# Optimization experiments

Hardware: AMD Instinct MI355X
Metric: run time of the kernel (lower is better)

Reference implementation:

```python
import jax, jax.numpy as jnp
import numpy as np

N = 50000          # nodes
E = 800000         # edges
D_IN, D_HID, D_OUT = 256, 128, 64
NUM_GRAPHS = 16
BN_EPS = 1e-5


def gcn_conv(x, src, dst, W, b, n_nodes):
    """PyG GCNConv: add self-loops, sym-normalized aggregation, then bias."""
    loop = jnp.arange(n_nodes, dtype=src.dtype)
    s = jnp.concatenate([src, loop])
    d = jnp.concatenate([dst, loop])
    deg = jax.ops.segment_sum(jnp.ones_like(s, dtype=x.dtype), d, num_segments=n_nodes)
    dinv = jax.lax.rsqrt(jnp.maximum(deg, 1.0))  # deg >= 1 due to self-loops
    norm = dinv[s] * dinv[d]                      # [E+N]
    h = x @ W                                     # [N, out]
    msg = h[s] * norm[:, None]                    # gather + scale
    out = jax.ops.segment_sum(msg, d, num_segments=n_nodes)
    return out + b


def batch_norm(x, gamma, beta):
    mu = jnp.mean(x, axis=0)
    var = jnp.mean(jnp.square(x - mu), axis=0)
    return (x - mu) * jax.lax.rsqrt(var + BN_EPS) * gamma + beta


def setup_inputs() -> dict:
    key = jax.random.key(0)
    ks = jax.random.split(key, 10)
    x = jax.random.normal(ks[0], (N, D_IN), dtype=jnp.float32)
    edge_index = jax.random.randint(ks[1], (2, E), 0, N, dtype=jnp.int64)
    batch = jnp.sort(jax.random.randint(ks[2], (N,), 0, NUM_GRAPHS, dtype=jnp.int64))
    def glorot(k, fan_in, fan_out):
        lim = np.sqrt(6.0 / (fan_in + fan_out))
        return jax.random.uniform(k, (fan_in, fan_out), jnp.float32, -lim, lim)
    return {
        "x": x, "edge_index": edge_index, "batch": batch,
        "W1": glorot(ks[3], D_IN, D_HID),  "b1": jnp.zeros((D_HID,), jnp.float32),
        "W2": glorot(ks[4], D_HID, D_HID), "b2": jnp.zeros((D_HID,), jnp.float32),
        "W3": glorot(ks[5], D_HID, D_OUT), "b3": jnp.zeros((D_OUT,), jnp.float32),
        "g1": jnp.ones((D_HID,), jnp.float32), "be1": jnp.zeros((D_HID,), jnp.float32),
        "g2": jnp.ones((D_HID,), jnp.float32), "be2": jnp.zeros((D_HID,), jnp.float32),
    }


def reference(x, edge_index, batch, W1, b1, W2, b2, W3, b3, g1, be1, g2, be2):
    src, dst = edge_index[0], edge_index[1]
    n = x.shape[0]
    h = gcn_conv(x, src, dst, W1, b1, n)
    h = jax.nn.relu(batch_norm(h, g1, be1))
    h = gcn_conv(h, src, dst, W2, b2, n)
    h = jax.nn.relu(batch_norm(h, g2, be2))
    h = gcn_conv(h, src, dst, W3, b3, n)          # [N, D_OUT]
    # global mean pool over graph ids
    sums = jax.ops.segment_sum(h, batch, num_segments=NUM_GRAPHS)
    cnts = jax.ops.segment_sum(jnp.ones((n,), h.dtype), batch, num_segments=NUM_GRAPHS)
    return sums / jnp.maximum(cnts, 1.0)[:, None]  # [NUM_GRAPHS, D_OUT]
```

## Files before the change

kernel.cpp:

```cpp
#include <hip/hip_runtime.h>
#include <hip/hip_bf16.h>

#define D_IN   256
#define D_HID  128
#define D_OUT_ 64
#define NGRAPH 16
#define BN_EPS 1e-5f

#define SCAN_TPB 256
#define SCAN_VPT 4

typedef __attribute__((ext_vector_type(8))) short short8;
typedef __attribute__((ext_vector_type(4))) float floatx4;

__device__ __forceinline__ unsigned short f2bf(float x) {
    unsigned u = __float_as_uint(x);
    return (unsigned short)((u + 0x7fffu + ((u >> 16) & 1u)) >> 16);
}
__device__ __forceinline__ unsigned pack2bf(float lo, float hi) {
    return (unsigned)f2bf(lo) | ((unsigned)f2bf(hi) << 16);
}
__device__ __forceinline__ void bf2_decode(unsigned u, float& lo, float& hi) {
    lo = __uint_as_float(u << 16);
    hi = __uint_as_float(u & 0xffff0000u);
}
__device__ __forceinline__ void accum8(float* acc, uint4 qv, float wt) {
    float f0,f1,f2,f3,f4,f5,f6,f7;
    bf2_decode(qv.x, f0, f1); bf2_decode(qv.y, f2, f3);
    bf2_decode(qv.z, f4, f5); bf2_decode(qv.w, f6, f7);
    acc[0]=fmaf(f0,wt,acc[0]); acc[1]=fmaf(f1,wt,acc[1]);
    acc[2]=fmaf(f2,wt,acc[2]); acc[3]=fmaf(f3,wt,acc[3]);
    acc[4]=fmaf(f4,wt,acc[4]); acc[5]=fmaf(f5,wt,acc[5]);
    acc[6]=fmaf(f6,wt,acc[6]); acc[7]=fmaf(f7,wt,acc[7]);
}

__global__ void count_rank_kernel(const int* __restrict__ dst, int E,
                                  int* __restrict__ deg, int* __restrict__ rank) {
    int e = blockIdx.x * blockDim.x + threadIdx.x;
    if (e < E) rank[e] = atomicAdd(&deg[dst[e]], 1);
}

__global__ void dinv_bsum_kernel(const int* __restrict__ deg, int N,
                                 float* __restrict__ dinv, int* __restrict__ bsum) {
    __shared__ int red[SCAN_TPB];
    int t = threadIdx.x;
    int base = blockIdx.x * (SCAN_TPB * SCAN_VPT) + t;
    int s = 0;
    #pragma unroll
    for (int i = 0; i < SCAN_VPT; ++i) {
        int idx = base + i * SCAN_TPB;
        if (idx < N) {
            int d = deg[idx];
            dinv[idx] = rsqrtf((float)(d + 1));
            s += d;
        }
    }
    red[t] = s;
    __syncthreads();
    for (int off = SCAN_TPB / 2; off > 0; off >>= 1) {
        if (t < off) red[t] += red[t + off];
        __syncthreads();
    }
    if (t == 0) bsum[blockIdx.x] = red[0];
}

__global__ void scan_bsum_kernel(const int* __restrict__ bsum, int NB,
                                 int* __restrict__ bprefix,
                                 int* __restrict__ rowstart, int N, int E) {
    __shared__ int part[SCAN_TPB];
    int t = threadIdx.x;
    int s = (t < NB) ? bsum[t] : 0;
    part[t] = s;
    __syncthreads();
    for (int off = 1; off < SCAN_TPB; off <<= 1) {
        int x = (t >= off) ? part[t - off] : 0;
        __syncthreads();
        part[t] += x;
        __syncthreads();
    }
    if (t < NB) bprefix[t] = part[t] - s;
    if (t == 0) rowstart[N] = E;
}

__global__ void local_scan_kernel(const int* __restrict__ deg, int N,
                                  const int* __restrict__ bprefix,
                                  int* __restrict__ rowstart) {
    __shared__ int part[SCAN_TPB];
    int t = threadIdx.x;
    int base = blockIdx.x * (SCAN_TPB * SCAN_VPT) + t * SCAN_VPT;
    int v[SCAN_VPT];
    int s = 0;
    #pragma unroll
    for (int i = 0; i < SCAN_VPT; ++i) {
        v[i] = (base + i < N) ? deg[base + i] : 0;
        s += v[i];
    }
    part[t] = s;
    __syncthreads();
    for (int off = 1; off < SCAN_TPB; off <<= 1) {
        int x = (t >= off) ? part[t - off] : 0;
        __syncthreads();
        part[t] += x;
        __syncthreads();
    }
    int excl = part[t] - s + bprefix[blockIdx.x];
    #pragma unroll
    for (int i = 0; i < SCAN_VPT; ++i) {
        if (base + i < N) rowstart[base + i] = excl;
        excl += v[i];
    }
}

__global__ void wprep_all_kernel(const float* __restrict__ W1, const float* __restrict__ W2,
                                 const float* __restrict__ W3,
                                 unsigned short* __restrict__ Wt1,
                                 unsigned short* __restrict__ Wt2,
                                 unsigned short* __restrict__ Wt3) {
    int idx = blockIdx.x * blockDim.x + threadIdx.x;
    const int S1 = D_IN * D_HID;
    const int S2 = D_HID * D_HID;
    const int S3 = D_HID * D_OUT_;
    if (idx < S1) {
        int k = idx / D_HID, n = idx - k * D_HID;
        Wt1[(size_t)n * D_IN + k] = f2bf(W1[idx]);
    } else if (idx < S1 + S2) {
        int i = idx - S1;
        int k = i / D_HID, n = i - k * D_HID;
        Wt2[(size_t)n * D_HID + k] = f2bf(W2[i]);
    } else if (idx < S1 + S2 + S3) {
        int i = idx - S1 - S2;
        int k = i / D_OUT_, n = i - k * D_OUT_;
        Wt3[(size_t)n * D_HID + k] = f2bf(W3[i]);
    }
}

template<int K, int NOUT, int FUSE, int ABF16>
__device__ __forceinline__ void gemm_body(
        int bid, const void* __restrict__ Aptr, const unsigned short* __restrict__ Wt,
        unsigned short* __restrict__ Cb, int M,
        const float* __restrict__ sums, const float* __restrict__ sumsq,
        const float* __restrict__ gam, const float* __restrict__ bet, float invN) {
    constexpr int NT = NOUT / 16;
    constexpr int KS = K / 32;
    __shared__ float s_sc[FUSE ? K : 1];
    __shared__ float s_sh[FUSE ? K : 1];
    if (FUSE) {
        int t = threadIdx.x;
        if (t < K) {
            float mu  = sums[t] * invN;
            float var = sumsq[t] * invN - mu * mu;
            float sc  = gam[t] * rsqrtf(var + BN_EPS);
            s_sc[t] = sc;
            s_sh[t] = fmaf(-mu, sc, bet[t]);
        }
        __syncthreads();
    }
    int lane = threadIdx.x & 63;
    int wave = threadIdx.x >> 6;
    int col  = lane & 15;
    int quad = lane >> 4;
    int kq   = quad * 8;
    int row  = bid * 64 + wave * 16 + col;
    int rowc = min(row, M - 1);

    short8 afr[KS];
    if (ABF16) {
        const unsigned short* Ab = (const unsigned short*)Aptr;
        uint4 q[KS];
        #pragma unroll
        for (int i = 0; i < KS; ++i)
            q[i] = *(const uint4*)&Ab[(size_t)rowc * K + i * 32 + kq];
        __builtin_amdgcn_sched_barrier(0);
        #pragma unroll
        for (int i = 0; i < KS; ++i) {
            if (FUSE) {
                int kb = i * 32 + kq;
                float f0,f1,f2,f3,f4,f5,f6,f7;
                bf2_decode(q[i].x, f0, f1); bf2_decode(q[i].y, f2, f3);
                bf2_decode(q[i].z, f4, f5); bf2_decode(q[i].w, f6, f7);
                float4 sc0 = *(const float4*)&s_sc[kb];
                float4 sc1 = *(const float4*)&s_sc[kb + 4];
                float4 sh0 = *(const float4*)&s_sh[kb];
                float4 sh1 = *(const float4*)&s_sh[kb + 4];
                f0 = fmaxf(0.f, fmaf(f0, sc0.x, sh0.x));
                f1 = fmaxf(0.f, fmaf(f1, sc0.y, sh0.y));
                f2 = fmaxf(0.f, fmaf(f2, sc0.z, sh0.z));
                f3 = fmaxf(0.f, fmaf(f3, sc0.w, sh0.w));
                f4 = fmaxf(0.f, fmaf(f4, sc1.x, sh1.x));
                f5 = fmaxf(0.f, fmaf(f5, sc1.y, sh1.y));
                f6 = fmaxf(0.f, fmaf(f6, sc1.z, sh1.z));
                f7 = fmaxf(0.f, fmaf(f7, sc1.w, sh1.w));
                uint4 p;
                p.x = pack2bf(f0, f1); p.y = pack2bf(f2, f3);
                p.z = pack2bf(f4, f5); p.w = pack2bf(f6, f7);
                afr[i] = __builtin_bit_cast(short8, p);
            } else {
                afr[i] = __builtin_bit_cast(short8, q[i]);
            }
        }
    } else {
        const float* Af = (const float*)Aptr;
        float4 a0[KS], a1[KS];
        #pragma unroll
        for (int i = 0; i < KS; ++i) {
            a0[i] = *(const float4*)&Af[(size_t)rowc * K + i * 32 + kq];
            a1[i] = *(const float4*)&Af[(size_t)rowc * K + i * 32 + kq + 4];
        }
        __builtin_amdgcn_sched_barrier(0);
        #pragma unroll
        for (int i = 0; i < KS; ++i) {
            uint4 p;
            p.x = pack2bf(a0[i].x, a0[i].y); p.y = pack2bf(a0[i].z, a0[i].w);
            p.z = pack2bf(a1[i].x, a1[i].y); p.w = pack2bf(a1[i].z, a1[i].w);
            afr[i] = __builtin_bit_cast(short8, p);
        }
    }

    floatx4 acc[NT];
    #pragma unroll
    for (int nt = 0; nt < NT; ++nt) acc[nt] = (floatx4){0.f, 0.f, 0.f, 0.f};

    #pragma unroll
    for (int i = 0; i < KS; ++i) {
        #pragma unroll
        for (int nt = 0; nt < NT; ++nt) {
            short8 bfrag = *(const short8*)&Wt[(size_t)(nt * 16 + col) * K + i * 32 + kq];
            acc[nt] = __builtin_amdgcn_mfma_f32_16x16x32_bf16(afr[i], bfrag, acc[nt], 0, 0, 0);
        }
    }

    int obase = bid * 64 + wave * 16 + quad * 4;
    #pragma unroll
    for (int r = 0; r < 4; ++r) {
        int orow = obase + r;
        if (orow < M) {
            #pragma unroll
            for (int nt = 0; nt < NT; ++nt)
                Cb[(size_t)orow * NOUT + nt * 16 + col] = f2bf(acc[nt][r]);
        }
    }
}

template<int K, int NOUT, int FUSE, int ABF16>
__global__ __launch_bounds__(256, 3) void gemm_mfma_kernel(
        const void* __restrict__ Aptr, const unsigned short* __restrict__ Wt,
        unsigned short* __restrict__ Cb, int M,
        const float* __restrict__ sums, const float* __restrict__ sumsq,
        const float* __restrict__ gam, const float* __restrict__ bet, float invN) {
    gemm_body<K, NOUT, FUSE, ABF16>(blockIdx.x, Aptr, Wt, Cb, M, sums, sumsq, gam, bet, invN);
}

__global__ __launch_bounds__(256, 3) void gemm1_scatter_kernel(
        const float* __restrict__ x, const unsigned short* __restrict__ Wt1,
        unsigned short* __restrict__ Cb, int M, int GB,
        const int* __restrict__ src, const int* __restrict__ dst, int E,
        const int* __restrict__ rowstart, const int* __restrict__ rank,
        int* __restrict__ csr) {
    if ((int)blockIdx.x < GB) {
        gemm_body<D_IN, D_HID, 0, 0>(blockIdx.x, x, Wt1, Cb, M,
                                     nullptr, nullptr, nullptr, nullptr, 0.f);
    } else {
        int e = ((int)blockIdx.x - GB) * 256 + threadIdx.x;
        if (e < E) {
            int d = dst[e];
            csr[rowstart[d] + rank[e]] = src[e];
        }
    }
}

template<int D>
__global__ __launch_bounds__(256) void agg_bf16_kernel(
        const unsigned short* __restrict__ h, const float* __restrict__ dinv,
        const int* __restrict__ rowstart, const int* __restrict__ csr,
        const float* __restrict__ bias,
        unsigned short* __restrict__ outb, int N) {
    constexpr int LPR = D / 8;
    constexpr int RPB = 256 / LPR;
    int lane = threadIdx.x & (LPR - 1);
    int r    = threadIdx.x / LPR;
    int v = blockIdx.x * RPB + r;
    if (v >= N) return;
    int c0 = lane * 8;
    const unsigned short* hc = h + c0;
    float dv = dinv[v];

    float acc[8];
    {
        float w = dv * dv;
        uint4 q = *(const uint4*)&hc[(size_t)v * D];
        float4 b0 = *(const float4*)&bias[c0];
        float4 b1 = *(const float4*)&bias[c0 + 4];
        acc[0]=b0.x; acc[1]=b0.y; acc[2]=b0.z; acc[3]=b0.w;
        acc[4]=b1.x; acc[5]=b1.y; acc[6]=b1.z; acc[7]=b1.w;
        accum8(acc, q, w);
    }

    int j  = rowstart[v];
    int j1 = rowstart[v + 1];
    for (; j + 8 <= j1; j += 8) {
        int   s[8]; float w[8]; uint4 q[8];
        #pragma unroll
        for (int i = 0; i < 8; ++i) s[i] = csr[j + i];
        #pragma unroll
        for (int i = 0; i < 8; ++i) q[i] = *(const uint4*)&hc[(size_t)s[i] * D];
        #pragma unroll
        for (int i = 0; i < 8; ++i) w[i] = dinv[s[i]] * dv;
        #pragma unroll
        for (int i = 0; i < 8; ++i) accum8(acc, q[i], w[i]);
    }
    for (; j + 4 <= j1; j += 4) {
        int s0 = csr[j],     s1 = csr[j + 1];
        int s2 = csr[j + 2], s3 = csr[j + 3];
        float w0 = dinv[s0] * dv, w1 = dinv[s1] * dv;
        float w2 = dinv[s2] * dv, w3 = dinv[s3] * dv;
        uint4 q0 = *(const uint4*)&hc[(size_t)s0 * D];
        uint4 q1 = *(const uint4*)&hc[(size_t)s1 * D];
        uint4 q2 = *(const uint4*)&hc[(size_t)s2 * D];
        uint4 q3 = *(const uint4*)&hc[(size_t)s3 * D];
        accum8(acc, q0, w0); accum8(acc, q1, w1);
        accum8(acc, q2, w2); accum8(acc, q3, w3);
    }
    for (; j < j1; ++j) {
        int s = csr[j];
        float w = dinv[s] * dv;
        uint4 q = *(const uint4*)&hc[(size_t)s * D];
        accum8(acc, q, w);
    }

    uint4 o;
    o.x = pack2bf(acc[0], acc[1]); o.y = pack2bf(acc[2], acc[3]);
    o.z = pack2bf(acc[4], acc[5]); o.w = pack2bf(acc[6], acc[7]);
    *(uint4*)&outb[(size_t)v * D + c0] = o;
}

__global__ void bn_stats_bf16_kernel(const unsigned short* __restrict__ x, int N,
                                     float* __restrict__ sums, float* __restrict__ sumsq) {
    __shared__ float ls0[256], ls1[256], lq0[256], lq1[256];
    int pr = threadIdx.x & 63;
    int rg = threadIdx.x >> 6;
    float s0=0.f, s1=0.f, q0=0.f, q1=0.f;
    for (int v = blockIdx.x * 4 + rg; v < N; v += gridDim.x * 4) {
        unsigned u = *(const unsigned*)&x[(size_t)v * 128 + pr * 2];
        float lo, hi; bf2_decode(u, lo, hi);
        s0 += lo; s1 += hi;
        q0 = fmaf(lo, lo, q0); q1 = fmaf(hi, hi, q1);
    }
    ls0[threadIdx.x]=s0; ls1[threadIdx.x]=s1; lq0[threadIdx.x]=q0; lq1[threadIdx.x]=q1;
    __syncthreads();
    if (threadIdx.x < 64) {
        int pp = threadIdx.x;
        float a0=0,a1=0,b0=0,b1=0;
        #pragma unroll
        for (int g = 0; g < 4; ++g) {
            a0 += ls0[g*64+pp]; a1 += ls1[g*64+pp];
            b0 += lq0[g*64+pp]; b1 += lq1[g*64+pp];
        }
        atomicAdd(&sums[pp*2],  a0); atomicAdd(&sums[pp*2+1],  a1);
        atomicAdd(&sumsq[pp*2], b0); atomicAdd(&sumsq[pp*2+1], b1);
    }
}

__global__ void pool_bf16_kernel(const unsigned short* __restrict__ x,
                                 const int* __restrict__ batch, int N,
                                 float* __restrict__ psum, int* __restrict__ pcnt) {
    __shared__ float ls[NGRAPH * 64];
    __shared__ int   lc[NGRAPH];
    for (int i = threadIdx.x; i < NGRAPH * 64; i += blockDim.x) ls[i] = 0.f;
    if (threadIdx.x < NGRAPH) lc[threadIdx.x] = 0;
    __syncthreads();
    int total = N * 32;
    for (int idx = blockIdx.x * blockDim.x + threadIdx.x; idx < total;
         idx += gridDim.x * blockDim.x) {
        int v = idx >> 5, cp = idx & 31;
        unsigned u = *(const unsigned*)&x[(size_t)v * 64 + cp * 2];
        float lo, hi; bf2_decode(u, lo, hi);
        int g = batch[v];
        atomicAdd(&ls[g * 64 + cp * 2],     lo);
        atomicAdd(&ls[g * 64 + cp * 2 + 1], hi);
        if (cp == 0) atomicAdd(&lc[g], 1);
    }
    __syncthreads();
    for (int i = threadIdx.x; i < NGRAPH * 64; i += blockDim.x) atomicAdd(&psum[i], ls[i]);
    if (threadIdx.x < NGRAPH) atomicAdd(&pcnt[threadIdx.x], lc[threadIdx.x]);
}

__global__ void pool_final_kernel(const float* __restrict__ psum, const int* __restrict__ pcnt,
                                  float* __restrict__ out) {
    int i = threadIdx.x;
    int g = i >> 6;
    float cnt = (float)max(pcnt[g], 1);
    out[i] = psum[i] / cnt;
}

extern "C" void kernel_launch(void* const* d_in, const int* in_sizes, int n_in,
                              void* d_out, int out_size, void* d_ws, size_t ws_size,
                              hipStream_t stream) {
    const float* x   = (const float*)d_in[0];
    const int*   ei  = (const int*)d_in[1];
    const int*   bat = (const int*)d_in[2];
    const float* W1  = (const float*)d_in[3];
    const float* b1  = (const float*)d_in[4];
    const float* W2  = (const float*)d_in[5];
    const float* b2  = (const float*)d_in[6];
    const float* W3  = (const float*)d_in[7];
    const float* b3  = (const float*)d_in[8];
    const float* g1  = (const float*)d_in[9];
    const float* be1 = (const float*)d_in[10];
    const float* g2  = (const float*)d_in[11];
    const float* be2 = (const float*)d_in[12];
    float* out = (float*)d_out;

    int N = in_sizes[0] / D_IN;
    int E = in_sizes[1] / 2;
    const int* src = ei;
    const int* dst = ei + E;

    char* p = (char*)d_ws;
    auto alloc = [&](size_t bytes) { char* r = p; p += (bytes + 255) & ~(size_t)255; return r; };
    int NB = (N + SCAN_TPB * SCAN_VPT - 1) / (SCAN_TPB * SCAN_VPT);
    char*  zbase    = p;
    int*   deg      = (int*)  alloc((size_t)N * 4);
    float* sums1    = (float*)alloc(128 * 4);
    float* sumsq1   = (float*)alloc(128 * 4);
    float* sums2    = (float*)alloc(128 * 4);
    float* sumsq2   = (float*)alloc(128 * 4);
    float* psum     = (float*)alloc(NGRAPH * 64 * 4);
    int*   pcnt     = (int*)  alloc(NGRAPH * 4);
    size_t zspan    = (size_t)(p - zbase);
    int*   rowstart = (int*)  alloc((size_t)(N + 1) * 4);
    int*   rank     = (int*)  alloc((size_t)E * 4);
    float* dinv     = (float*)alloc((size_t)N * 4);
    int*   bsum     = (int*)  alloc((size_t)NB * 4);
    int*   bprefix  = (int*)  alloc((size_t)NB * 4);
    int*   csr      = (int*)  alloc((size_t)E * 4);
    unsigned short* hb16   = (unsigned short*)alloc((size_t)N * 128 * 2);
    unsigned short* aggb16 = (unsigned short*)alloc((size_t)N * 128 * 2);
    unsigned short* Wt1 = (unsigned short*)alloc((size_t)D_HID * D_IN * 2);
    unsigned short* Wt2 = (unsigned short*)alloc((size_t)D_HID * D_HID * 2);
    unsigned short* Wt3 = (unsigned short*)alloc((size_t)D_OUT_ * D_HID * 2);

    int tpb = 256;
    int ebl = (E + tpb - 1) / tpb;
    int gblocks = (N + 63) / 64;
    float invN = 1.0f / (float)N;
    int wtot = D_IN * D_HID + D_HID * D_HID + D_HID * D_OUT_;

    (void)hipMemsetAsync(zbase, 0, zspan, stream);
    wprep_all_kernel<<<(wtot + 255) / 256, 256, 0, stream>>>(W1, W2, W3, Wt1, Wt2, Wt3);

    count_rank_kernel<<<ebl, tpb, 0, stream>>>(dst, E, deg, rank);
    dinv_bsum_kernel<<<NB, SCAN_TPB, 0, stream>>>(deg, N, dinv, bsum);
    scan_bsum_kernel<<<1, SCAN_TPB, 0, stream>>>(bsum, NB, bprefix, rowstart, N, E);
    local_scan_kernel<<<NB, SCAN_TPB, 0, stream>>>(deg, N, bprefix, rowstart);

    gemm1_scatter_kernel<<<gblocks + ebl, 256, 0, stream>>>(
        x, Wt1, hb16, N, gblocks, src, dst, E, rowstart, rank, csr);

    agg_bf16_kernel<D_HID><<<(N + 15) / 16, 256, 0, stream>>>(
        hb16, dinv, rowstart, csr, b1, aggb16, N);
    bn_stats_bf16_kernel<<<256, 256, 0, stream>>>(aggb16, N, sums1, sumsq1);

    gemm_mfma_kernel<D_HID, D_HID, 1, 1><<<gblocks, 256, 0, stream>>>(
        aggb16, Wt2, hb16, N, sums1, sumsq1, g1, be1, invN);
    agg_bf16_kernel<D_HID><<<(N + 15) / 16, 256, 0, stream>>>(
        hb16, dinv, rowstart, csr, b2, aggb16, N);
    bn_stats_bf16_kernel<<<256, 256, 0, stream>>>(aggb16, N, sums2, sumsq2);

    gemm_mfma_kernel<D_HID, D_OUT_, 1, 1><<<gblocks, 256, 0, stream>>>(
        aggb16, Wt3, hb16, N, sums2, sumsq2, g2, be2, invN);
    agg_bf16_kernel<D_OUT_><<<(N + 31) / 32, 256, 0, stream>>>(
        hb16, dinv, rowstart, csr, b3, aggb16, N);

    pool_bf16_kernel<<<256, 256, 0, stream>>>(aggb16, bat, N, psum, pcnt);
    pool_final_kernel<<<1, NGRAPH * 64, 0, stream>>>(psum, pcnt, out);
}
```

Measured before the change: 385.8 us.

## Fuse whole GCN pipeline into one cooperative persistent kernel with grid syncs

Replaces the chain of roughly fourteen kernel launches with a single cooperative persistent kernel. Each former kernel becomes a stage in a grid-stride loop, and stages are separated by grid.sync(). This removes per-launch overhead and the idle gaps between small kernels. In exchange, the kernel is limited to an occupancy-sized grid with launch bounds of 4 blocks per CU, so register pressure may hurt the GEMM and aggregation stages. Each of the roughly thirteen grid barriers also has its own cost. The old multi-kernel path is kept as a fallback if the cooperative launch fails.

```diff
diff --git a/kernel.cpp b/kernel.cpp
--- a/kernel.cpp
+++ b/kernel.cpp
@@ -1,14 +1,14 @@
 #include <hip/hip_runtime.h>
 #include <hip/hip_bf16.h>
+#include <hip/hip_cooperative_groups.h>
+
+namespace cg = cooperative_groups;
 
 #define D_IN   256
 #define D_HID  128
 #define D_OUT_ 64
 #define NGRAPH 16
 #define BN_EPS 1e-5f
-
-#define SCAN_TPB 256
-#define SCAN_VPT 4
 
 typedef __attribute__((ext_vector_type(8))) short short8;
 typedef __attribute__((ext_vector_type(4))) float floatx4;
@@ -34,118 +34,18 @@
     acc[6]=fmaf(f6,wt,acc[6]); acc[7]=fmaf(f7,wt,acc[7]);
 }
 
-__global__ void count_rank_kernel(const int* __restrict__ dst, int E,
-                                  int* __restrict__ deg, int* __restrict__ rank) {
-    int e = blockIdx.x * blockDim.x + threadIdx.x;
-    if (e < E) rank[e] = atomicAdd(&deg[dst[e]], 1);
-}
-
-__global__ void dinv_bsum_kernel(const int* __restrict__ deg, int N,
-                                 float* __restrict__ dinv, int* __restrict__ bsum) {
-    __shared__ int red[SCAN_TPB];
-    int t = threadIdx.x;
-    int base = blockIdx.x * (SCAN_TPB * SCAN_VPT) + t;
-    int s = 0;
-    #pragma unroll
-    for (int i = 0; i < SCAN_VPT; ++i) {
-        int idx = base + i * SCAN_TPB;
-        if (idx < N) {
-            int d = deg[idx];
-            dinv[idx] = rsqrtf((float)(d + 1));
-            s += d;
-        }
-    }
-    red[t] = s;
-    __syncthreads();
-    for (int off = SCAN_TPB / 2; off > 0; off >>= 1) {
-        if (t < off) red[t] += red[t + off];
-        __syncthreads();
-    }
-    if (t == 0) bsum[blockIdx.x] = red[0];
-}
-
-__global__ void scan_bsum_kernel(const int* __restrict__ bsum, int NB,
-                                 int* __restrict__ bprefix,
-                                 int* __restrict__ rowstart, int N, int E) {
-    __shared__ int part[SCAN_TPB];
-    int t = threadIdx.x;
-    int s = (t < NB) ? bsum[t] : 0;
-    part[t] = s;
-    __syncthreads();
-    for (int off = 1; off < SCAN_TPB; off <<= 1) {
-        int x = (t >= off) ? part[t - off] : 0;
-        __syncthreads();
-        part[t] += x;
-        __syncthreads();
-    }
-    if (t < NB) bprefix[t] = part[t] - s;
-    if (t == 0) rowstart[N] = E;
-}
-
-__global__ void local_scan_kernel(const int* __restrict__ deg, int N,
-                                  const int* __restrict__ bprefix,
-                                  int* __restrict__ rowstart) {
-    __shared__ int part[SCAN_TPB];
-    int t = threadIdx.x;
-    int base = blockIdx.x * (SCAN_TPB * SCAN_VPT) + t * SCAN_VPT;
-    int v[SCAN_VPT];
-    int s = 0;
-    #pragma unroll
-    for (int i = 0; i < SCAN_VPT; ++i) {
-        v[i] = (base + i < N) ? deg[base + i] : 0;
-        s += v[i];
-    }
-    part[t] = s;
-    __syncthreads();
-    for (int off = 1; off < SCAN_TPB; off <<= 1) {
-        int x = (t >= off) ? part[t - off] : 0;
-        __syncthreads();
-        part[t] += x;
-        __syncthreads();
-    }
-    int excl = part[t] - s + bprefix[blockIdx.x];
-    #pragma unroll
-    for (int i = 0; i < SCAN_VPT; ++i) {
-        if (base + i < N) rowstart[base + i] = excl;
-        excl += v[i];
-    }
-}
-
-__global__ void wprep_all_kernel(const float* __restrict__ W1, const float* __restrict__ W2,
-                                 const float* __restrict__ W3,
-                                 unsigned short* __restrict__ Wt1,
-                                 unsigned short* __restrict__ Wt2,
-                                 unsigned short* __restrict__ Wt3) {
-    int idx = blockIdx.x * blockDim.x + threadIdx.x;
-    const int S1 = D_IN * D_HID;
-    const int S2 = D_HID * D_HID;
-    const int S3 = D_HID * D_OUT_;
-    if (idx < S1) {
-        int k = idx / D_HID, n = idx - k * D_HID;
-        Wt1[(size_t)n * D_IN + k] = f2bf(W1[idx]);
-    } else if (idx < S1 + S2) {
-        int i = idx - S1;
-        int k = i / D_HID, n = i - k * D_HID;
-        Wt2[(size_t)n * D_HID + k] = f2bf(W2[i]);
-    } else if (idx < S1 + S2 + S3) {
-        int i = idx - S1 - S2;
-        int k = i / D_OUT_, n = i - k * D_OUT_;
-        Wt3[(size_t)n * D_HID + k] = f2bf(W3[i]);
-    }
-}
-
 template<int K, int NOUT, int FUSE, int ABF16>
 __device__ __forceinline__ void gemm_body(
         int bid, const void* __restrict__ Aptr, const unsigned short* __restrict__ Wt,
         unsigned short* __restrict__ Cb, int M,
         const float* __restrict__ sums, const float* __restrict__ sumsq,
-        const float* __restrict__ gam, const float* __restrict__ bet, float invN) {
+        const float* __restrict__ gam, const float* __restrict__ bet, float invN,
+        float* s_sc, float* s_sh) {
     constexpr int NT = NOUT / 16;
     constexpr int KS = K / 32;
-    __shared__ float s_sc[FUSE ? K : 1];
-    __shared__ float s_sh[FUSE ? K : 1];
     if (FUSE) {
         int t = threadIdx.x;
+        __syncthreads();
         if (t < K) {
             float mu  = sums[t] * invN;
             float var = sumsq[t] * invN - mu * mu;
@@ -241,48 +141,20 @@
     }
 }
 
-template<int K, int NOUT, int FUSE, int ABF16>
-__global__ __launch_bounds__(256, 3) void gemm_mfma_kernel(
-        const void* __restrict__ Aptr, const unsigned short* __restrict__ Wt,
-        unsigned short* __restrict__ Cb, int M,
-        const float* __restrict__ sums, const float* __restrict__ sumsq,
-        const float* __restrict__ gam, const float* __restrict__ bet, float invN) {
-    gemm_body<K, NOUT, FUSE, ABF16>(blockIdx.x, Aptr, Wt, Cb, M, sums, sumsq, gam, bet, invN);
-}
-
-__global__ __launch_bounds__(256, 3) void gemm1_scatter_kernel(
-        const float* __restrict__ x, const unsigned short* __restrict__ Wt1,
-        unsigned short* __restrict__ Cb, int M, int GB,
-        const int* __restrict__ src, const int* __restrict__ dst, int E,
-        const int* __restrict__ rowstart, const int* __restrict__ rank,
-        int* __restrict__ csr) {
-    if ((int)blockIdx.x < GB) {
-        gemm_body<D_IN, D_HID, 0, 0>(blockIdx.x, x, Wt1, Cb, M,
-                                     nullptr, nullptr, nullptr, nullptr, 0.f);
-    } else {
-        int e = ((int)blockIdx.x - GB) * 256 + threadIdx.x;
-        if (e < E) {
-            int d = dst[e];
-            csr[rowstart[d] + rank[e]] = src[e];
-        }
-    }
-}
-
 template<int D>
-__global__ __launch_bounds__(256) void agg_bf16_kernel(
-        const unsigned short* __restrict__ h, const float* __restrict__ dinv,
+__device__ __forceinline__ void agg_tile(
+        int tile, const unsigned short* __restrict__ h, const float* __restrict__ dinvp,
         const int* __restrict__ rowstart, const int* __restrict__ csr,
-        const float* __restrict__ bias,
-        unsigned short* __restrict__ outb, int N) {
+        const float* __restrict__ bias, unsigned short* __restrict__ outb, int N) {
     constexpr int LPR = D / 8;
     constexpr int RPB = 256 / LPR;
     int lane = threadIdx.x & (LPR - 1);
     int r    = threadIdx.x / LPR;
-    int v = blockIdx.x * RPB + r;
+    int v = tile * RPB + r;
     if (v >= N) return;
     int c0 = lane * 8;
     const unsigned short* hc = h + c0;
-    float dv = dinv[v];
+    float dv = dinvp[v];
 
     float acc[8];
     {
@@ -294,7 +166,6 @@
         acc[4]=b1.x; acc[5]=b1.y; acc[6]=b1.z; acc[7]=b1.w;
         accum8(acc, q, w);
     }
-
     int j  = rowstart[v];
     int j1 = rowstart[v + 1];
     for (; j + 8 <= j1; j += 8) {
@@ -304,15 +175,15 @@
         #pragma unroll
         for (int i = 0; i < 8; ++i) q[i] = *(const uint4*)&hc[(size_t)s[i] * D];
         #pragma unroll
-        for (int i = 0; i < 8; ++i) w[i] = dinv[s[i]] * dv;
+        for (int i = 0; i < 8; ++i) w[i] = dinvp[s[i]] * dv;
         #pragma unroll
         for (int i = 0; i < 8; ++i) accum8(acc, q[i], w[i]);
     }
     for (; j + 4 <= j1; j += 4) {
         int s0 = csr[j],     s1 = csr[j + 1];
         int s2 = csr[j + 2], s3 = csr[j + 3];
-        float w0 = dinv[s0] * dv, w1 = dinv[s1] * dv;
-        float w2 = dinv[s2] * dv, w3 = dinv[s3] * dv;
+        float w0 = dinvp[s0] * dv, w1 = dinvp[s1] * dv;
+        float w2 = dinvp[s2] * dv, w3 = dinvp[s3] * dv;
         uint4 q0 = *(const uint4*)&hc[(size_t)s0 * D];
         uint4 q1 = *(const uint4*)&hc[(size_t)s1 * D];
         uint4 q2 = *(const uint4*)&hc[(size_t)s2 * D];
@@ -322,42 +193,353 @@
     }
     for (; j < j1; ++j) {
         int s = csr[j];
-        float w = dinv[s] * dv;
+        float w = dinvp[s] * dv;
         uint4 q = *(const uint4*)&hc[(size_t)s * D];
         accum8(acc, q, w);
     }
-
     uint4 o;
     o.x = pack2bf(acc[0], acc[1]); o.y = pack2bf(acc[2], acc[3]);
     o.z = pack2bf(acc[4], acc[5]); o.w = pack2bf(acc[6], acc[7]);
     *(uint4*)&outb[(size_t)v * D + c0] = o;
 }
 
-__global__ void bn_stats_bf16_kernel(const unsigned short* __restrict__ x, int N,
-                                     float* __restrict__ sums, float* __restrict__ sumsq) {
-    __shared__ float ls0[256], ls1[256], lq0[256], lq1[256];
-    int pr = threadIdx.x & 63;
-    int rg = threadIdx.x >> 6;
+__device__ __forceinline__ void bn_stats_body(
+        const unsigned short* __restrict__ x, int N,
+        float* __restrict__ sums, float* __restrict__ sumsq, float* sm, int G) {
+    float* ls0 = sm; float* ls1 = sm + 256; float* lq0 = sm + 512; float* lq1 = sm + 768;
+    int tid = threadIdx.x;
+    int pr = tid & 63, rg = tid >> 6;
     float s0=0.f, s1=0.f, q0=0.f, q1=0.f;
-    for (int v = blockIdx.x * 4 + rg; v < N; v += gridDim.x * 4) {
+    for (int v = (int)blockIdx.x * 4 + rg; v < N; v += G * 4) {
         unsigned u = *(const unsigned*)&x[(size_t)v * 128 + pr * 2];
         float lo, hi; bf2_decode(u, lo, hi);
         s0 += lo; s1 += hi;
         q0 = fmaf(lo, lo, q0); q1 = fmaf(hi, hi, q1);
     }
-    ls0[threadIdx.x]=s0; ls1[threadIdx.x]=s1; lq0[threadIdx.x]=q0; lq1[threadIdx.x]=q1;
     __syncthreads();
-    if (threadIdx.x < 64) {
-        int pp = threadIdx.x;
+    ls0[tid]=s0; ls1[tid]=s1; lq0[tid]=q0; lq1[tid]=q1;
+    __syncthreads();
+    if (tid < 64) {
         float a0=0,a1=0,b0=0,b1=0;
         #pragma unroll
         for (int g = 0; g < 4; ++g) {
-            a0 += ls0[g*64+pp]; a1 += ls1[g*64+pp];
-            b0 += lq0[g*64+pp]; b1 += lq1[g*64+pp];
-        }
-        atomicAdd(&sums[pp*2],  a0); atomicAdd(&sums[pp*2+1],  a1);
-        atomicAdd(&sumsq[pp*2], b0); atomicAdd(&sumsq[pp*2+1], b1);
-    }
+            a0 += ls0[g*64+tid]; a1 += ls1[g*64+tid];
+            b0 += lq0[g*64+tid]; b1 += lq1[g*64+tid];
+        }
+        atomicAdd(&sums[tid*2],  a0); atomicAdd(&sums[tid*2+1],  a1);
+        atomicAdd(&sumsq[tid*2], b0); atomicAdd(&sumsq[tid*2+1], b1);
+    }
+}
+
+struct MegaParams {
+    const float* x;
+    const int* src; const int* dst; const int* batch;
+    const float *W1,*b1,*W2,*b2,*W3,*b3,*g1,*be1,*g2,*be2;
+    float* out;
+    int N, E, NB, gblocks, ebl, aggT128, aggT64;
+    float invN;
+    int* deg; int* rowstart; int* rank; float* dinvp; int* bsum; int* csr;
+    unsigned short *hb16, *aggb16, *Wt1, *Wt2, *Wt3;
+    float *sums1,*sumsq1,*sums2,*sumsq2,*psum; int* pcnt;
+};
+
+__global__ __launch_bounds__(256, 4) void mega_kernel(MegaParams P) {
+    cg::grid_group grid = cg::this_grid();
+    __shared__ float smf[1024];
+    __shared__ int   smi[256];
+    int tid   = threadIdx.x;
+    int b     = blockIdx.x;
+    int G     = gridDim.x;
+    int gtid  = b * 256 + tid;
+    int gsize = G * 256;
+
+    {
+        const int S1 = D_IN * D_HID, S2 = D_HID * D_HID, S3 = D_HID * D_OUT_;
+        for (int idx = gtid; idx < S1 + S2 + S3; idx += gsize) {
+            if (idx < S1) {
+                int k = idx / D_HID, n = idx - k * D_HID;
+                P.Wt1[(size_t)n * D_IN + k] = f2bf(P.W1[idx]);
+            } else if (idx < S1 + S2) {
+                int i = idx - S1; int k = i / D_HID, n = i - k * D_HID;
+                P.Wt2[(size_t)n * D_HID + k] = f2bf(P.W2[i]);
+            } else {
+                int i = idx - S1 - S2; int k = i / D_OUT_, n = i - k * D_OUT_;
+                P.Wt3[(size_t)n * D_HID + k] = f2bf(P.W3[i]);
+            }
+        }
+        for (int e = gtid; e < P.E; e += gsize)
+            P.rank[e] = atomicAdd(&P.deg[P.dst[e]], 1);
+    }
+    grid.sync();
+
+    for (int i = gtid; i < P.N; i += gsize)
+        P.dinvp[i] = rsqrtf((float)(P.deg[i] + 1));
+    for (int t = b; t < P.NB; t += G) {
+        int base = t * 1024 + tid;
+        int s = 0;
+        #pragma unroll
+        for (int i = 0; i < 4; ++i) {
+            int idx = base + i * 256;
+            if (idx < P.N) s += P.deg[idx];
+        }
+        __syncthreads();
+        smi[tid] = s;
+        __syncthreads();
+        for (int off = 128; off > 0; off >>= 1) {
+            if (tid < off) smi[tid] += smi[tid + off];
+            __syncthreads();
+        }
+        if (tid == 0) P.bsum[t] = smi[0];
+    }
+    grid.sync();
+
+    if (b == 0 && tid == 0) P.rowstart[P.N] = P.E;
+    for (int t = b; t < P.NB; t += G) {
+        int val = (tid < t) ? P.bsum[tid] : 0;
+        __syncthreads();
+        smi[tid] = val;
+        __syncthreads();
+        for (int off = 128; off > 0; off >>= 1) {
+            if (tid < off) smi[tid] += smi[tid + off];
+            __syncthreads();
+        }
+        int bpref = smi[0];
+        __syncthreads();
+        int base = t * 1024 + tid * 4;
+        int v[4]; int s = 0;
+        #pragma unroll
+        for (int i = 0; i < 4; ++i) {
+            v[i] = (base + i < P.N) ? P.deg[base + i] : 0;
+            s += v[i];
+        }
+        smi[tid] = s;
+        __syncthreads();
+        for (int off = 1; off < 256; off <<= 1) {
+            int x2 = (tid >= off) ? smi[tid - off] : 0;
+            __syncthreads();
+            smi[tid] += x2;
+            __syncthreads();
+        }
+        int excl = smi[tid] - s + bpref;
+        #pragma unroll
+        for (int i = 0; i < 4; ++i) {
+            if (base + i < P.N) P.rowstart[base + i] = excl;
+            excl += v[i];
+        }
+    }
+    grid.sync();
+
+    for (int t = b; t < P.gblocks; t += G)
+        gemm_body<D_IN, D_HID, 0, 0>(t, P.x, P.Wt1, P.hb16, P.N,
+                                     nullptr, nullptr, nullptr, nullptr, 0.f,
+                                     smf, smf + 128);
+    for (int c = b; c < P.ebl; c += G) {
+        int e = c * 256 + tid;
+        if (e < P.E) {
+            int d = P.dst[e];
+            P.csr[P.rowstart[d] + P.rank[e]] = P.src[e];
+        }
+    }
+    grid.sync();
+
+    for (int t = b; t < P.aggT128; t += G)
+        agg_tile<D_HID>(t, P.hb16, P.dinvp, P.rowstart, P.csr, P.b1, P.aggb16, P.N);
+    grid.sync();
+
+    bn_stats_body(P.aggb16, P.N, P.sums1, P.sumsq1, smf, G);
+    grid.sync();
+
+    for (int t = b; t < P.gblocks; t += G)
+        gemm_body<D_HID, D_HID, 1, 1>(t, P.aggb16, P.Wt2, P.hb16, P.N,
+                                      P.sums1, P.sumsq1, P.g1, P.be1, P.invN,
+                                      smf, smf + 128);
+    grid.sync();
+
+    for (int t = b; t < P.aggT128; t += G)
+        agg_tile<D_HID>(t, P.hb16, P.dinvp, P.rowstart, P.csr, P.b2, P.aggb16, P.N);
+    grid.sync();
+
+    bn_stats_body(P.aggb16, P.N, P.sums2, P.sumsq2, smf, G);
+    grid.sync();
+
+    for (int t = b; t < P.gblocks; t += G)
+        gemm_body<D_HID, D_OUT_, 1, 1>(t, P.aggb16, P.Wt3, P.hb16, P.N,
+                                       P.sums2, P.sumsq2, P.g2, P.be2, P.invN,
+                                       smf, smf + 128);
+    grid.sync();
+
+    for (int t = b; t < P.aggT64; t += G)
+        agg_tile<D_OUT_>(t, P.hb16, P.dinvp, P.rowstart, P.csr, P.b3, P.aggb16, P.N);
+    grid.sync();
+
+    {
+        __syncthreads();
+        for (int i = tid; i < NGRAPH * 64; i += 256) smf[i] = 0.f;
+        if (tid < NGRAPH) smi[tid] = 0;
+        __syncthreads();
+        int total = P.N * 32;
+        for (int idx = gtid; idx < total; idx += gsize) {
+            int v = idx >> 5, cp = idx & 31;
+            unsigned u = *(const unsigned*)&P.aggb16[(size_t)v * 64 + cp * 2];
+            float lo, hi; bf2_decode(u, lo, hi);
+            int g = P.batch[v];
+            atomicAdd(&smf[g * 64 + cp * 2],     lo);
+            atomicAdd(&smf[g * 64 + cp * 2 + 1], hi);
+            if (cp == 0) atomicAdd(&smi[g], 1);
+        }
+        __syncthreads();
+        for (int i = tid; i < NGRAPH * 64; i += 256) atomicAdd(&P.psum[i], smf[i]);
+        if (tid < NGRAPH) atomicAdd(&P.pcnt[tid], smi[tid]);
+    }
+    grid.sync();
+
+    if (b == 0) {
+        for (int i = tid; i < NGRAPH * 64; i += 256) {
+            int g = i >> 6;
+            P.out[i] = P.psum[i] / (float)max(P.pcnt[g], 1);
+        }
+    }
+}
+
+__global__ void count_rank_kernel(const int* __restrict__ dst, int E,
+                                  int* __restrict__ deg, int* __restrict__ rank) {
+    int e = blockIdx.x * blockDim.x + threadIdx.x;
+    if (e < E) rank[e] = atomicAdd(&deg[dst[e]], 1);
+}
+
+__global__ void dinv_bsum_kernel(const int* __restrict__ deg, int N,
+                                 float* __restrict__ dinvp, int* __restrict__ bsum) {
+    __shared__ int red[256];
+    int t = threadIdx.x;
+    int base = blockIdx.x * 1024 + t;
+    int s = 0;
+    #pragma unroll
+    for (int i = 0; i < 4; ++i) {
+        int idx = base + i * 256;
+        if (idx < N) {
+            int d = deg[idx];
+            dinvp[idx] = rsqrtf((float)(d + 1));
+            s += d;
+        }
+    }
+    red[t] = s;
+    __syncthreads();
+    for (int off = 128; off > 0; off >>= 1) {
+        if (t < off) red[t] += red[t + off];
+        __syncthreads();
+    }
+    if (t == 0) bsum[blockIdx.x] = red[0];
+}
+
+__global__ void scan_bsum_kernel(const int* __restrict__ bsum, int NB,
+                                 int* __restrict__ bprefix,
+                                 int* __restrict__ rowstart, int N, int E) {
+    __shared__ int part[256];
+    int t = threadIdx.x;
+    int s = (t < NB) ? bsum[t] : 0;
+    part[t] = s;
+    __syncthreads();
+    for (int off = 1; off < 256; off <<= 1) {
+        int x = (t >= off) ? part[t - off] : 0;
+        __syncthreads();
+        part[t] += x;
+        __syncthreads();
+    }
+    if (t < NB) bprefix[t] = part[t] - s;
+    if (t == 0) rowstart[N] = E;
+}
+
+__global__ void local_scan_kernel(const int* __restrict__ deg, int N,
+                                  const int* __restrict__ bprefix,
+                                  int* __restrict__ rowstart) {
+    __shared__ int part[256];
+    int t = threadIdx.x;
+    int base = blockIdx.x * 1024 + t * 4;
+    int v[4]; int s = 0;
+    #pragma unroll
+    for (int i = 0; i < 4; ++i) {
+        v[i] = (base + i < N) ? deg[base + i] : 0;
+        s += v[i];
+    }
+    part[t] = s;
+    __syncthreads();
+    for (int off = 1; off < 256; off <<= 1) {
+        int x = (t >= off) ? part[t - off] : 0;
+        __syncthreads();
+        part[t] += x;
+        __syncthreads();
+    }
+    int excl = part[t] - s + bprefix[blockIdx.x];
+    #pragma unroll
+    for (int i = 0; i < 4; ++i) {
+        if (base + i < N) rowstart[base + i] = excl;
+        excl += v[i];
+    }
+}
+
+__global__ void wprep_all_kernel(const float* __restrict__ W1, const float* __restrict__ W2,
+                                 const float* __restrict__ W3,
+                                 unsigned short* __restrict__ Wt1,
+                                 unsigned short* __restrict__ Wt2,
+                                 unsigned short* __restrict__ Wt3) {
+    int idx = blockIdx.x * blockDim.x + threadIdx.x;
+    const int S1 = D_IN * D_HID, S2 = D_HID * D_HID, S3 = D_HID * D_OUT_;
+    if (idx < S1) {
+        int k = idx / D_HID, n = idx - k * D_HID;
+        Wt1[(size_t)n * D_IN + k] = f2bf(W1[idx]);
+    } else if (idx < S1 + S2) {
+        int i = idx - S1; int k = i / D_HID, n = i - k * D_HID;
+        Wt2[(size_t)n * D_HID + k] = f2bf(W2[i]);
+    } else if (idx < S1 + S2 + S3) {
+        int i = idx - S1 - S2; int k = i / D_OUT_, n = i - k * D_OUT_;
+        Wt3[(size_t)n * D_HID + k] = f2bf(W3[i]);
+    }
+}
+
+template<int K, int NOUT, int FUSE, int ABF16>
+__global__ __launch_bounds__(256, 3) void gemm_mfma_kernel(
+        const void* __restrict__ Aptr, const unsigned short* __restrict__ Wt,
+        unsigned short* __restrict__ Cb, int M,
+        const float* __restrict__ sums, const float* __restrict__ sumsq,
+        const float* __restrict__ gam, const float* __restrict__ bet, float invN) {
+    __shared__ float s_sc[FUSE ? K : 1];
+    __shared__ float s_sh[FUSE ? K : 1];
+    gemm_body<K, NOUT, FUSE, ABF16>(blockIdx.x, Aptr, Wt, Cb, M,
+                                    sums, sumsq, gam, bet, invN, s_sc, s_sh);
+}
+
+__global__ __launch_bounds__(256, 3) void gemm1_scatter_kernel(
+        const float* __restrict__ x, const unsigned short* __restrict__ Wt1,
+        unsigned short* __restrict__ Cb, int M, int GB,
+        const int* __restrict__ src, const int* __restrict__ dst, int E,
+        const int* __restrict__ rowstart, const int* __restrict__ rank,
+        int* __restrict__ csr) {
+    if ((int)blockIdx.x < GB) {
+        gemm_body<D_IN, D_HID, 0, 0>(blockIdx.x, x, Wt1, Cb, M,
+                                     nullptr, nullptr, nullptr, nullptr, 0.f,
+                                     nullptr, nullptr);
+    } else {
+        int e = ((int)blockIdx.x - GB) * 256 + threadIdx.x;
+        if (e < E) {
+            int d = dst[e];
+            csr[rowstart[d] + rank[e]] = src[e];
+        }
+    }
+}
+
+template<int D>
+__global__ __launch_bounds__(256) void agg_bf16_kernel(
+        const unsigned short* __restrict__ h, const float* __restrict__ dinvp,
+        const int* __restrict__ rowstart, const int* __restrict__ csr,
+        const float* __restrict__ bias,
+        unsigned short* __restrict__ outb, int N) {
+    agg_tile<D>(blockIdx.x, h, dinvp, rowstart, csr, bias, outb, N);
+}
+
+__global__ void bn_stats_bf16_kernel(const unsigned short* __restrict__ x, int N,
+                                     float* __restrict__ sums, float* __restrict__ sumsq) {
+    __shared__ float sm[1024];
+    bn_stats_body(x, N, sums, sumsq, sm, gridDim.x);
 }
 
 __global__ void pool_bf16_kernel(const unsigned short* __restrict__ x,
@@ -395,82 +577,95 @@
 extern "C" void kernel_launch(void* const* d_in, const int* in_sizes, int n_in,
                               void* d_out, int out_size, void* d_ws, size_t ws_size,
                               hipStream_t stream) {
-    const float* x   = (const float*)d_in[0];
-    const int*   ei  = (const int*)d_in[1];
-    const int*   bat = (const int*)d_in[2];
-    const float* W1  = (const float*)d_in[3];
-    const float* b1  = (const float*)d_in[4];
-    const float* W2  = (const float*)d_in[5];
-    const float* b2  = (const float*)d_in[6];
-    const float* W3  = (const float*)d_in[7];
-    const float* b3  = (const float*)d_in[8];
-    const float* g1  = (const float*)d_in[9];
-    const float* be1 = (const float*)d_in[10];
-    const float* g2  = (const float*)d_in[11];
-    const float* be2 = (const float*)d_in[12];
-    float* out = (float*)d_out;
-
-    int N = in_sizes[0] / D_IN;
-    int E = in_sizes[1] / 2;
-    const int* src = ei;
-    const int* dst = ei + E;
+    MegaParams P;
+    P.x   = (const float*)d_in[0];
+    const int* ei = (const int*)d_in[1];
+    P.batch = (const int*)d_in[2];
+    P.W1  = (const float*)d_in[3];  P.b1  = (const float*)d_in[4];
+    P.W2  = (const float*)d_in[5];  P.b2  = (const float*)d_in[6];
+    P.W3  = (const float*)d_in[7];  P.b3  = (const float*)d_in[8];
+    P.g1  = (const float*)d_in[9];  P.be1 = (const float*)d_in[10];
+    P.g2  = (const float*)d_in[11]; P.be2 = (const float*)d_in[12];
+    P.out = (float*)d_out;
+
+    P.N = in_sizes[0] / D_IN;
+    P.E = in_sizes[1] / 2;
+    P.src = ei;
+    P.dst = ei + P.E;
+    P.NB      = (P.N + 1023) / 1024;
+    P.gblocks = (P.N + 63) / 64;
+    P.ebl     = (P.E + 255) / 256;
+    P.aggT128 = (P.N + 15) / 16;
+    P.aggT64  = (P.N + 31) / 32;
+    P.invN    = 1.0f / (float)P.N;
 
     char* p = (char*)d_ws;
     auto alloc = [&](size_t bytes) { char* r = p; p += (bytes + 255) & ~(size_t)255; return r; };
-    int NB = (N + SCAN_TPB * SCAN_VPT - 1) / (SCAN_TPB * SCAN_VPT);
-    char*  zbase    = p;
-    int*   deg      = (int*)  alloc((size_t)N * 4);
-    float* sums1    = (float*)alloc(128 * 4);
-    float* sumsq1   = (float*)alloc(128 * 4);
-    float* sums2    = (float*)alloc(128 * 4);
-    float* sumsq2   = (float*)alloc(128 * 4);
-    float* psum     = (float*)alloc(NGRAPH * 64 * 4);
-    int*   pcnt     = (int*)  alloc(NGRAPH * 4);
-    size_t zspan    = (size_t)(p - zbase);
-    int*   rowstart = (int*)  alloc((size_t)(N + 1) * 4);
-    int*   rank     = (int*)  alloc((size_t)E * 4);
-    float* dinv     = (float*)alloc((size_t)N * 4);
-    int*   bsum     = (int*)  alloc((size_t)NB * 4);
-    int*   bprefix  = (int*)  alloc((size_t)NB * 4);
-    int*   csr      = (int*)  alloc((size_t)E * 4);
-    unsigned short* hb16   = (unsigned short*)alloc((size_t)N * 128 * 2);
-    unsigned short* aggb16 = (unsigned short*)alloc((size_t)N * 128 * 2);
-    unsigned short* Wt1 = (unsigned short*)alloc((size_t)D_HID * D_IN * 2);
-    unsigned short* Wt2 = (unsigned short*)alloc((size_t)D_HID * D_HID * 2);
-    unsigned short* Wt3 = (unsigned short*)alloc((size_t)D_OUT_ * D_HID * 2);
-
-    int tpb = 256;
-    int ebl = (E + tpb - 1) / tpb;
-    int gblocks = (N + 63) / 64;
-    float invN = 1.0f / (float)N;
-    int wtot = D_IN * D_HID + D_HID * D_HID + D_HID * D_OUT_;
+    char* zbase = p;
+    P.deg    = (int*)  alloc((size_t)P.N * 4);
+    P.sums1  = (float*)alloc(128 * 4);
+    P.sumsq1 = (float*)alloc(128 * 4);
+    P.sums2  = (float*)alloc(128 * 4);
+    P.sumsq2 = (float*)alloc(128 * 4);
+    P.psum   = (float*)alloc(NGRAPH * 64 * 4);
+    P.pcnt   = (int*)  alloc(NGRAPH * 4);
+    size_t zspan = (size_t)(p - zbase);
+    P.rowstart = (int*)  alloc((size_t)(P.N + 1) * 4);
+    P.rank     = (int*)  alloc((size_t)P.E * 4);
+    P.dinvp    = (float*)alloc((size_t)P.N * 4);
+    P.bsum     = (int*)  alloc((size_t)P.NB * 4);
+    int* bprefix = (int*)alloc((size_t)P.NB * 4);
+    P.csr      = (int*)  alloc((size_t)P.E * 4);
+    P.hb16     = (unsigned short*)alloc((size_t)P.N * 128 * 2);
+    P.aggb16   = (unsigned short*)alloc((size_t)P.N * 128 * 2);
+    P.Wt1      = (unsigned short*)alloc((size_t)D_HID * D_IN * 2);
+    P.Wt2      = (unsigned short*)alloc((size_t)D_HID * D_HID * 2);
+    P.Wt3      = (unsigned short*)alloc((size_t)D_OUT_ * D_HID * 2);
 
     (void)hipMemsetAsync(zbase, 0, zspan, stream);
-    wprep_all_kernel<<<(wtot + 255) / 256, 256, 0, stream>>>(W1, W2, W3, Wt1, Wt2, Wt3);
-
-    count_rank_kernel<<<ebl, tpb, 0, stream>>>(dst, E, deg, rank);
-    dinv_bsum_kernel<<<NB, SCAN_TPB, 0, stream>>>(deg, N, dinv, bsum);
-    scan_bsum_kernel<<<1, SCAN_TPB, 0, stream>>>(bsum, NB, bprefix, rowstart, N, E);
-    local_scan_kernel<<<NB, SCAN_TPB, 0, stream>>>(deg, N, bprefix, rowstart);
-
-    gemm1_scatter_kernel<<<gblocks + ebl, 256, 0, stream>>>(
-        x, Wt1, hb16, N, gblocks, src, dst, E, rowstart, rank, csr);
-
-    agg_bf16_kernel<D_HID><<<(N + 15) / 16, 256, 0, stream>>>(
-        hb16, dinv, rowstart, csr, b1, aggb16, N);
-    bn_stats_bf16_kernel<<<256, 256, 0, stream>>>(aggb16, N, sums1, sumsq1);
-
-    gemm_mfma_kernel<D_HID, D_HID, 1, 1><<<gblocks, 256, 0, stream>>>(
-        aggb16, Wt2, hb16, N, sums1, sumsq1, g1, be1, invN);
-    agg_bf16_kernel<D_HID><<<(N + 15) / 16, 256, 0, stream>>>(
-        hb16, dinv, rowstart, csr, b2, aggb16, N);
-    bn_stats_bf16_kernel<<<256, 256, 0, stream>>>(aggb16, N, sums2, sumsq2);
-
-    gemm_mfma_kernel<D_HID, D_OUT_, 1, 1><<<gblocks, 256, 0, stream>>>(
-        aggb16, Wt3, hb16, N, sums2, sumsq2, g2, be2, invN);
-    agg_bf16_kernel<D_OUT_><<<(N + 31) / 32, 256, 0, stream>>>(
-        hb16, dinv, rowstart, csr, b3, aggb16, N);
-
-    pool_bf16_kernel<<<256, 256, 0, stream>>>(aggb16, bat, N, psum, pcnt);
-    pool_final_kernel<<<1, NGRAPH * 64, 0, stream>>>(psum, pcnt, out);
-}
+
+    int occ = 0;
+    hipError_t oerr = hipOccupancyMaxActiveBlocksPerMultiprocessor(&occ, mega_kernel, 256, 0);
+    int nCU = 256;
+    hipDeviceProp_t props;
+    int dev = 0;
+    if (hipGetDevice(&dev) == hipSuccess &&
+        hipGetDeviceProperties(&props, dev) == hipSuccess)
+        nCU = props.multiProcessorCount;
+
+    bool coop_ok = false;
+    if (oerr == hipSuccess && occ >= 1) {
+        int grid = occ * nCU;
+        void* kargs[] = { (void*)&P };
+        hipError_t lerr = hipLaunchCooperativeKernel((const void*)mega_kernel,
+                                                     dim3(grid), dim3(256), kargs, 0, stream);
+        if (lerr == hipSuccess) coop_ok = true;
+        else (void)hipGetLastError();
+    }
+
+    if (!coop_ok) {
+        int gblocks = P.gblocks;
+        count_rank_kernel<<<P.ebl, 256, 0, stream>>>(P.dst, P.E, P.deg, P.rank);
+        dinv_bsum_kernel<<<P.NB, 256, 0, stream>>>(P.deg, P.N, P.dinvp, P.bsum);
+        scan_bsum_kernel<<<1, 256, 0, stream>>>(P.bsum, P.NB, bprefix, P.rowstart, P.N, P.E);
+        local_scan_kernel<<<P.NB, 256, 0, stream>>>(P.deg, P.N, bprefix, P.rowstart);
+        wprep_all_kernel<<<(D_IN*D_HID + D_HID*D_HID + D_HID*D_OUT_ + 255) / 256, 256, 0,
+                          stream>>>(P.W1, P.W2, P.W3, P.Wt1, P.Wt2, P.Wt3);
+        gemm1_scatter_kernel<<<gblocks + P.ebl, 256, 0, stream>>>(
+            P.x, P.Wt1, P.hb16, P.N, gblocks, P.src, P.dst, P.E, P.rowstart, P.rank, P.csr);
+        agg_bf16_kernel<D_HID><<<P.aggT128, 256, 0, stream>>>(
+            P.hb16, P.dinvp, P.rowstart, P.csr, P.b1, P.aggb16, P.N);
+        bn_stats_bf16_kernel<<<256, 256, 0, stream>>>(P.aggb16, P.N, P.sums1, P.sumsq1);
+        gemm_mfma_kernel<D_HID, D_HID, 1, 1><<<gblocks, 256, 0, stream>>>(
+            P.aggb16, P.Wt2, P.hb16, P.N, P.sums1, P.sumsq1, P.g1, P.be1, P.invN);
+        agg_bf16_kernel<D_HID><<<P.aggT128, 256, 0, stream>>>(
+            P.hb16, P.dinvp, P.rowstart, P.csr, P.b2, P.aggb16, P.N);
+        bn_stats_bf16_kernel<<<256, 256, 0, stream>>>(P.aggb16, P.N, P.sums2, P.sumsq2);
+        gemm_mfma_kernel<D_HID, D_OUT_, 1, 1><<<gblocks, 256, 0, stream>>>(
+            P.aggb16, P.Wt3, P.hb16, P.N, P.sums2, P.sumsq2, P.g2, P.be2, P.invN);
+        agg_bf16_kernel<D_OUT_><<<P.aggT64, 256, 0, stream>>>(
+            P.hb16, P.dinvp, P.rowstart, P.csr, P.b3, P.aggb16, P.N);
+        pool_bf16_kernel<<<256, 256, 0, stream>>>(P.aggb16, P.batch, P.N, P.psum, P.pcnt);
+        pool_final_kernel<<<1, NGRAPH * 64, 0, stream>>>(P.psum, P.pcnt, P.out);
+    }
+}
```

Measured after the change: 1.116 ms. 189% more time.
